# Kernel optimization log

Hardware: AMD Instinct MI355X
Metric: run time of the kernel (lower is better)

Reference implementation:

```python
import jax, jax.numpy as jnp
import numpy as np


def setup_inputs() -> dict:
    key = jax.random.key(0)
    ks = jax.random.split(key, 8)
    C = 256
    x = jax.random.normal(ks[0], (8, C, 64, 64), dtype=jnp.float32)
    scale = 1.0 / np.sqrt(C)
    Wb = jax.random.normal(ks[1], (C, C), dtype=jnp.float32) * scale
    bb = jax.random.normal(ks[2], (C,), dtype=jnp.float32) * 0.01
    Wc = jax.random.normal(ks[3], (C, C), dtype=jnp.float32) * scale
    bc = jax.random.normal(ks[4], (C,), dtype=jnp.float32) * 0.01
    Wd = jax.random.normal(ks[5], (C, C), dtype=jnp.float32) * scale
    bd = jax.random.normal(ks[6], (C,), dtype=jnp.float32) * 0.01
    alpha = jnp.zeros((1,), dtype=jnp.float32) + 0.1  # nonzero so output depends on attention path
    return {"x": x, "Wb": Wb, "bb": bb, "Wc": Wc, "bc": bc, "Wd": Wd, "bd": bd, "alpha": alpha}


def _pam(x, Wb, bb, Wc, bc, Wd, bd, alpha):
    n, c, h, w = x.shape
    xf = x.reshape(n, c, h * w)  # [n, c, N]
    # 1x1 conv == per-pixel linear over channels: W @ x + b
    B = jnp.einsum('oc,ncl->nlo', Wb, xf) + bb  # [n, N, c]
    Cm = jnp.einsum('oc,ncl->nol', Wc, xf) + bc[None, :, None]  # [n, c, N]
    D = jnp.einsum('oc,ncl->nlo', Wd, xf) + bd  # [n, N, c]
    attn = jax.nn.softmax(jnp.einsum('nic,ncj->nij', B, Cm), axis=-1)  # [n, N, N]
    y = jnp.einsum('nij,njc->nic', attn, D)  # [n, N, c]
    y = y.transpose(0, 2, 1).reshape(n, c, h, w)
    return alpha * y + x


def reference(x, Wb, bb, Wc, bc, Wd, bd, alpha):
    return _pam(x, Wb, bb, Wc, bc, Wd, bd, alpha)
```

## Files before the change

kernel.cpp:

```cpp
#include <hip/hip_runtime.h>

using bf16x8 = __attribute__((ext_vector_type(8))) short;
using f32x4  = __attribute__((ext_vector_type(4))) float;
using f32x16 = __attribute__((ext_vector_type(16))) float;
using u32x4  = __attribute__((ext_vector_type(4))) unsigned int;

#define NPIX 4096
#define CCH  256

__device__ __forceinline__ unsigned short f2bf(float f) {
  unsigned int u = __builtin_bit_cast(unsigned int, f);
  u += 0x7FFFu + ((u >> 16) & 1u);
  return (unsigned short)(u >> 16);
}

__device__ __forceinline__ float bfu(unsigned short h) {
  unsigned int u = ((unsigned int)h) << 16;
  return __builtin_bit_cast(float, u);
}

__device__ __forceinline__ unsigned int pack2(float a, float b) {
  return (unsigned int)f2bf(a) | ((unsigned int)f2bf(b) << 16);
}

__device__ __forceinline__ void gld_lds16(const void* g, void* l) {
  __builtin_amdgcn_global_load_lds(
      (const __attribute__((address_space(1))) unsigned int*)g,
      (__attribute__((address_space(3))) unsigned int*)l, 16, 0, 0);
}

__global__ __launch_bounds__(256) void convert_w_kernel(
    const float* __restrict__ Wb, const float* __restrict__ Wc,
    const float* __restrict__ Wd, unsigned short* __restrict__ Wbf) {
  const int mat = blockIdx.y;
  const float* src = (mat == 0) ? Wb : (mat == 1) ? Wc : Wd;
  int i = (blockIdx.x * 256 + threadIdx.x) * 4;
  float4 v = *reinterpret_cast<const float4*>(src + i);
  uint2 o;
  o.x = pack2(v.x, v.y);
  o.y = pack2(v.z, v.w);
  *reinterpret_cast<uint2*>(Wbf + mat * 65536 + i) = o;
}

__global__ __launch_bounds__(256, 2) void fused_proj_kernel(
    const float* __restrict__ x, const unsigned short* __restrict__ Wbf,
    const float* __restrict__ bb, const float* __restrict__ bc,
    const float* __restrict__ bd, unsigned short* __restrict__ Q,
    unsigned short* __restrict__ K, unsigned short* __restrict__ Vt) {
  __shared__ __align__(16) float tile[64][65];
  __shared__ __align__(16) char xsub[32768];
  char* bounce = (char*)tile;

  const int tid = threadIdx.x;
  const int wid = tid >> 6, lane = tid & 63;
  const int l31 = lane & 31, hi = lane >> 5;
  const int lt = blockIdx.x, n = blockIdx.y;

  #pragma unroll 1
  for (int ct = 0; ct < 4; ++ct) {
    const float* xg = x + ((size_t)(n * CCH + ct * 64)) * NPIX + lt * 64;
    #pragma unroll
    for (int it = 0; it < 4; ++it) {
      int row = (tid >> 4) + it * 16;
      int col = (tid & 15) * 4;
      float4 v = *reinterpret_cast<const float4*>(xg + (size_t)row * NPIX + col);
      tile[row][col] = v.x; tile[row][col + 1] = v.y;
      tile[row][col + 2] = v.z; tile[row][col + 3] = v.w;
    }
    __syncthreads();
    #pragma unroll
    for (int it = 0; it < 2; ++it) {
      int idx = tid + it * 256;
      int l = idx >> 3;
      int ch = (idx & 7) * 8;
      int c = ct * 64 + ch;
      uint4 o;
      o.x = pack2(tile[ch + 0][l], tile[ch + 1][l]);
      o.y = pack2(tile[ch + 2][l], tile[ch + 3][l]);
      o.z = pack2(tile[ch + 4][l], tile[ch + 5][l]);
      o.w = pack2(tile[ch + 6][l], tile[ch + 7][l]);
      int addr = (l >> 5) * 16384 + (c >> 4) * 1024 + ((c >> 3) & 1) * 512 + (l & 31) * 16;
      *reinterpret_cast<uint4*>(xsub + addr) = o;
    }
    __syncthreads();
  }

  const int o0a = wid * 64, o0b = wid * 64 + 32;
  const size_t pixrow = (size_t)n * NPIX + lt * 64;

  #pragma unroll 1
  for (int mat = 0; mat < 3; ++mat) {
    const unsigned short* W = Wbf + mat * 65536;
    const float* bias = (mat == 0) ? bb : (mat == 1) ? bc : bd;
    f32x16 a00, a01, a10, a11;
    #pragma unroll
    for (int e = 0; e < 16; ++e) { a00[e] = 0.f; a01[e] = 0.f; a10[e] = 0.f; a11[e] = 0.f; }
    #pragma unroll
    for (int c0 = 0; c0 < 16; ++c0) {
      bf16x8 x0 = *reinterpret_cast<const bf16x8*>(xsub + c0 * 1024 + lane * 16);
      bf16x8 x1 = *reinterpret_cast<const bf16x8*>(xsub + 16384 + c0 * 1024 + lane * 16);
      bf16x8 w0 = *reinterpret_cast<const bf16x8*>(W + (o0a + l31) * CCH + c0 * 16 + hi * 8);
      bf16x8 w1 = *reinterpret_cast<const bf16x8*>(W + (o0b + l31) * CCH + c0 * 16 + hi * 8);
      if (mat < 2) {
        a00 = __builtin_amdgcn_mfma_f32_32x32x16_bf16(w0, x0, a00, 0, 0, 0);
        a01 = __builtin_amdgcn_mfma_f32_32x32x16_bf16(w0, x1, a01, 0, 0, 0);
        a10 = __builtin_amdgcn_mfma_f32_32x32x16_bf16(w1, x0, a10, 0, 0, 0);
        a11 = __builtin_amdgcn_mfma_f32_32x32x16_bf16(w1, x1, a11, 0, 0, 0);
      } else {
        a00 = __builtin_amdgcn_mfma_f32_32x32x16_bf16(x0, w0, a00, 0, 0, 0);
        a01 = __builtin_amdgcn_mfma_f32_32x32x16_bf16(x1, w0, a01, 0, 0, 0);
        a10 = __builtin_amdgcn_mfma_f32_32x32x16_bf16(x0, w1, a10, 0, 0, 0);
        a11 = __builtin_amdgcn_mfma_f32_32x32x16_bf16(x1, w1, a11, 0, 0, 0);
      }
    }
    if (mat < 2) {
      unsigned short* dst = (mat == 0) ? Q : K;
      #pragma unroll 1
      for (int ph = 0; ph < 2; ++ph) {
        __syncthreads();
        const f32x16& A0 = ph ? a01 : a00;
        const f32x16& A1 = ph ? a11 : a10;
        const int swz = (l31 & 15) << 4;
        #pragma unroll
        for (int r2 = 0; r2 < 8; ++r2) {
          const int r = r2 * 2;
          const int od = (r & 3) + 8 * (r >> 2) + 4 * hi;
          const int oa = o0a + od, ob = o0b + od;
          *reinterpret_cast<unsigned int*>(bounce + ((l31 * 512 + oa * 2) ^ swz)) =
              pack2(A0[r] + bias[oa], A0[r + 1] + bias[oa + 1]);
          *reinterpret_cast<unsigned int*>(bounce + ((l31 * 512 + ob * 2) ^ swz)) =
              pack2(A1[r] + bias[ob], A1[r + 1] + bias[ob + 1]);
        }
        __syncthreads();
        const int dp = tid >> 3, obase = (tid & 7) * 32;
        const int dswz = (dp & 15) << 4;
        char* gout = (char*)(dst + (pixrow + ph * 32 + dp) * CCH + obase);
        #pragma unroll
        for (int k = 0; k < 4; ++k) {
          u32x4 v = *reinterpret_cast<const u32x4*>(
              bounce + ((dp * 512 + obase * 2 + k * 16) ^ dswz));
          *reinterpret_cast<u32x4*>(gout + k * 16) = v;
        }
      }
    } else {
      #pragma unroll 1
      for (int os = 0; os < 2; ++os) {
        __syncthreads();
        if ((wid >> 1) == os) {
          const int ola = o0a + l31 - os * 128, olb = o0b + l31 - os * 128;
          const float bva = bias[o0a + l31], bvb = bias[o0b + l31];
          const int sza = (ola & 7) << 4, szb = (olb & 7) << 4;
          #pragma unroll
          for (int r2 = 0; r2 < 8; ++r2) {
            const int r = r2 * 2;
            const int pd = (r & 3) + 8 * (r >> 2) + 4 * hi;
            *reinterpret_cast<unsigned int*>(bounce + ((ola * 128 + pd * 2) ^ sza)) =
                pack2(a00[r] + bva, a00[r + 1] + bva);
            *reinterpret_cast<unsigned int*>(bounce + ((ola * 128 + (pd + 32) * 2) ^ sza)) =
                pack2(a01[r] + bva, a01[r + 1] + bva);
            *reinterpret_cast<unsigned int*>(bounce + ((olb * 128 + pd * 2) ^ szb)) =
                pack2(a10[r] + bvb, a10[r + 1] + bvb);
            *reinterpret_cast<unsigned int*>(bounce + ((olb * 128 + (pd + 32) * 2) ^ szb)) =
                pack2(a11[r] + bvb, a11[r + 1] + bvb);
          }
        }
        __syncthreads();
        const int ol = tid >> 1, pb0 = (tid & 1) * 32;
        const int vswz = (ol & 7) << 4;
        char* gout = (char*)(Vt + ((size_t)(n * CCH + os * 128 + ol)) * NPIX + lt * 64 + pb0);
        #pragma unroll
        for (int k = 0; k < 4; ++k) {
          u32x4 v = *reinterpret_cast<const u32x4*>(
              bounce + ((ol * 128 + pb0 * 2 + k * 16) ^ vswz));
          *reinterpret_cast<u32x4*>(gout + k * 16) = v;
        }
      }
    }
  }
}

__global__ __launch_bounds__(256, 2) void attn_part_kernel(
    const unsigned short* __restrict__ Q, const unsigned short* __restrict__ K,
    const unsigned short* __restrict__ Vt, unsigned short* __restrict__ Opart,
    float* __restrict__ lsumbuf) {
  __shared__ __align__(16) char smem[65536];

  const int tid = threadIdx.x;
  const int wid = tid >> 6;
  const int lane = tid & 63;
  const int l31 = lane & 31;
  const int hi = lane >> 5;
  const int lofs = lane << 4;
  const int blk = blockIdx.x;
  const int n = blk & 7;
  const int t2 = blk >> 3;
  const int half = t2 & 1;
  const int qb = t2 >> 1;
  const int q0 = qb * 128 + wid * 32;

  const unsigned short* Qg = Q + (size_t)n * NPIX * CCH;
  const char* Kg = (const char*)(K + ((size_t)n * NPIX + half * 2048) * CCH);
  const char* Vg = (const char*)(Vt + (size_t)n * CCH * NPIX + half * 2048);

  bf16x8 qf[16];
  #pragma unroll
  for (int c0 = 0; c0 < 16; ++c0)
    qf[c0] = *reinterpret_cast<const bf16x8*>(
        Qg + (size_t)(q0 + l31) * CCH + c0 * 16 + hi * 8);

  f32x16 oacc[8];
  #pragma unroll
  for (int i = 0; i < 8; ++i)
    #pragma unroll
    for (int e = 0; e < 16; ++e) oacc[i][e] = 0.f;
  float lsum = 0.f;

  const bool isK = wid < 2;
  const char* splane = isK ? Kg : Vg;
  const int sinc = isK ? 32 * 512 : 64;
  int soff[8];
  #pragma unroll
  for (int g = 0; g < 8; ++g) {
    int s = ((wid & 1) << 3) + g;
    if (isK) {
      soff[g] = l31 * 512 + s * 32 + hi * 16;
    } else {
      int cb = s >> 1, kk2 = s & 1;
      soff[g] = (cb * 32 + l31) * 8192 + (kk2 * 16 + hi * 8) * 2;
    }
  }

  auto STAGE = [&](int par, int adv) {
    #pragma unroll
    for (int g = 0; g < 8; ++g)
      gld_lds16(splane + (size_t)soff[g] + (size_t)adv,
                smem + par * 32768 + (((wid << 3) + g) << 10));
  };

  STAGE(0, 0);
  __syncthreads();

  #pragma unroll 1
  for (int t = 0; t < 64; ++t) {
    const int par = t & 1;
    const char* kb = smem + par * 32768;
    const char* vb = kb + 16384;

    f32x16 S;
    #pragma unroll
    for (int e = 0; e < 16; ++e) S[e] = 0.f;
    __builtin_amdgcn_s_setprio(1);
    #pragma unroll
    for (int c0 = 0; c0 < 16; ++c0) {
      bf16x8 kf = *reinterpret_cast<const bf16x8*>(kb + c0 * 1024 + lofs);
      S = __builtin_amdgcn_mfma_f32_32x32x16_bf16(kf, qf[c0], S, 0, 0, 0);
    }
    __builtin_amdgcn_s_setprio(0);

    if (t < 63) STAGE(par ^ 1, (t + 1) * sinc);

    float rsum = 0.f;
    unsigned int pw[8];
    #pragma unroll
    for (int i = 0; i < 8; ++i) {
      float p0 = exp2f(fmaf(S[2 * i],     1.44269504f, -101.0f));
      float p1 = exp2f(fmaf(S[2 * i + 1], 1.44269504f, -101.0f));
      rsum += p0 + p1;
      unsigned int r;
      asm("v_cvt_pk_bf16_f32 %0, %1, %2" : "=v"(r) : "v"(p0), "v"(p1));
      pw[i] = r;
    }
    lsum += rsum;

    unsigned int s0a = pw[0], s0b = pw[2];
    unsigned int s1a = pw[1], s1b = pw[3];
    unsigned int s2a = pw[4], s2b = pw[6];
    unsigned int s3a = pw[5], s3b = pw[7];
    asm volatile("v_permlane32_swap_b32 %0, %1" : "+v"(s0a), "+v"(s0b));
    asm volatile("v_permlane32_swap_b32 %0, %1" : "+v"(s1a), "+v"(s1b));
    asm volatile("v_permlane32_swap_b32 %0, %1" : "+v"(s2a), "+v"(s2b));
    asm volatile("v_permlane32_swap_b32 %0, %1" : "+v"(s3a), "+v"(s3b));
    u32x4 f0, f1;
    f0[0] = s0a; f0[1] = s1a; f0[2] = s0b; f0[3] = s1b;
    f1[0] = s2a; f1[1] = s3a; f1[2] = s2b; f1[3] = s3b;
    bf16x8 pa0 = __builtin_bit_cast(bf16x8, f0);
    bf16x8 pa1 = __builtin_bit_cast(bf16x8, f1);

    __builtin_amdgcn_s_setprio(1);
    #pragma unroll
    for (int cb = 0; cb < 8; ++cb) {
      bf16x8 v0 = *reinterpret_cast<const bf16x8*>(vb + (cb * 2 + 0) * 1024 + lofs);
      oacc[cb] = __builtin_amdgcn_mfma_f32_32x32x16_bf16(pa0, v0, oacc[cb], 0, 0, 0);
      bf16x8 v1 = *reinterpret_cast<const bf16x8*>(vb + (cb * 2 + 1) * 1024 + lofs);
      oacc[cb] = __builtin_amdgcn_mfma_f32_32x32x16_bf16(pa1, v1, oacc[cb], 0, 0, 0);
    }
    __builtin_amdgcn_s_setprio(0);

    __syncthreads();
  }

  lsum += __shfl_xor(lsum, 32);
  char* slab = (char*)Opart + (size_t)blk * 65536;
  #pragma unroll
  for (int cb = 0; cb < 8; ++cb) {
    u32x4 u0, u1;
    u0[0] = pack2(oacc[cb][0],  oacc[cb][1]);
    u0[1] = pack2(oacc[cb][2],  oacc[cb][3]);
    u0[2] = pack2(oacc[cb][4],  oacc[cb][5]);
    u0[3] = pack2(oacc[cb][6],  oacc[cb][7]);
    u1[0] = pack2(oacc[cb][8],  oacc[cb][9]);
    u1[1] = pack2(oacc[cb][10], oacc[cb][11]);
    u1[2] = pack2(oacc[cb][12], oacc[cb][13]);
    u1[3] = pack2(oacc[cb][14], oacc[cb][15]);
    *reinterpret_cast<u32x4*>(slab + (cb * 2 + 0) * 4096 + tid * 16) = u0;
    *reinterpret_cast<u32x4*>(slab + (cb * 2 + 1) * 4096 + tid * 16) = u1;
  }
  if (hi == 0) lsumbuf[blk * 128 + wid * 32 + l31] = lsum;
}

__global__ __launch_bounds__(512) void merge_kernel(
    const unsigned short* __restrict__ Opart, const float* __restrict__ lsumbuf,
    const float* __restrict__ x, const float* __restrict__ alpha_p,
    float* __restrict__ out) {
  __shared__ float T[32768];
  __shared__ float Lq[128];

  const int tid = threadIdx.x;
  const int pr8 = tid >> 6;
  const int lane = tid & 63;
  const int l31 = lane & 31;
  const int hi = lane >> 5;
  const int qsub = pr8 & 3;
  const int cbh = pr8 >> 2;
  const int atid = qsub * 64 + lane;
  const int m = blockIdx.x;
  const int n = m & 7;
  const int qb = m >> 3;
  const int blkA = n + 8 * (0 + 2 * qb);
  const int blkB = n + 8 * (1 + 2 * qb);

  if (tid < 128)
    Lq[tid] = alpha_p[0] / (lsumbuf[blkA * 128 + tid] + lsumbuf[blkB * 128 + tid]);
  __syncthreads();

  const char* sa = (const char*)Opart + (size_t)blkA * 65536;
  const char* sb = (const char*)Opart + (size_t)blkB * 65536;

  #pragma unroll
  for (int cbi = 0; cbi < 4; ++cbi) {
    const int cb = cbh * 4 + cbi;
    const int c = cb * 32 + l31;
    const int swz = c & 28;
    #pragma unroll
    for (int h = 0; h < 2; ++h) {
      u32x4 a = *reinterpret_cast<const u32x4*>(sa + (cb * 2 + h) * 4096 + atid * 16);
      u32x4 b = *reinterpret_cast<const u32x4*>(sb + (cb * 2 + h) * 4096 + atid * 16);
      #pragma unroll
      for (int w = 0; w < 4; ++w) {
        const int r = h * 8 + w * 2;
        float v0 = bfu((unsigned short)(a[w] & 0xFFFF)) + bfu((unsigned short)(b[w] & 0xFFFF));
        float v1 = bfu((unsigned short)(a[w] >> 16)) + bfu((unsigned short)(b[w] >> 16));
        const int q0l = qsub * 32 + ((r) & 3) + 8 * ((r) >> 2) + 4 * hi;
        const int q1l = q0l + 1;
        T[c * 128 + (q0l ^ swz)] = v0 * Lq[q0l];
        T[c * 128 + (q1l ^ swz)] = v1 * Lq[q1l];
      }
    }
  }
  __syncthreads();

  const int l0 = (tid & 31) * 4;
  #pragma unroll 4
  for (int sw = 0; sw < 16; ++sw) {
    const int c = (tid >> 5) + sw * 16;
    const float* src = &T[c * 128 + (l0 ^ (c & 28))];
    float4 v = *reinterpret_cast<const float4*>(src);
    const size_t g = ((size_t)n * CCH + c) * NPIX + qb * 128 + l0;
    float4 xi = *reinterpret_cast<const float4*>(x + g);
    float4 o;
    o.x = v.x + xi.x; o.y = v.y + xi.y; o.z = v.z + xi.z; o.w = v.w + xi.w;
    *reinterpret_cast<float4*>(out + g) = o;
  }
}

extern "C" void kernel_launch(void* const* d_in, const int* in_sizes, int n_in,
                              void* d_out, int out_size, void* d_ws, size_t ws_size,
                              hipStream_t stream) {
  const float* x  = (const float*)d_in[0];
  const float* Wb = (const float*)d_in[1];
  const float* bb = (const float*)d_in[2];
  const float* Wc = (const float*)d_in[3];
  const float* bc = (const float*)d_in[4];
  const float* Wd = (const float*)d_in[5];
  const float* bd = (const float*)d_in[6];
  const float* alpha = (const float*)d_in[7];
  float* out = (float*)d_out;
  char* ws = (char*)d_ws;

  unsigned short* Wbf   = (unsigned short*)(ws);
  unsigned short* Q     = (unsigned short*)(ws + 393216);
  unsigned short* K     = (unsigned short*)(ws + 17170432);
  unsigned short* Vt    = (unsigned short*)(ws + 33947648);
  unsigned short* Opart = (unsigned short*)(ws + 50724864);
  float*          lsumb = (float*)(ws + 84279296);

  convert_w_kernel<<<dim3(64, 3), 256, 0, stream>>>(Wb, Wc, Wd, Wbf);
  fused_proj_kernel<<<dim3(64, 8), 256, 0, stream>>>(x, Wbf, bb, bc, bd, Q, K, Vt);
  attn_part_kernel<<<dim3(512), 256, 0, stream>>>(Q, K, Vt, Opart, lsumb);
  merge_kernel<<<dim3(256), 512, 0, stream>>>(Opart, lsumb, x, alpha, out);
}
```

Measured before the change: 215.1 us.

## Split K/V staging across all waves with finer-grained vmcnt pipelining

Every wave now loads a share of both the K and the V tiles, instead of two waves loading K and two loading V. The next tile's K is prefetched at the top of each iteration and its V after the QK MFMAs. The single end-of-iteration __syncthreads is replaced by two s_waitcnt vmcnt(8) plus s_barrier points placed just before QK and just before PV, so each phase waits only for the data it consumes. This aims to overlap global-to-LDS transfers more deeply with compute, at the cost of one redundant wrapped tile load per block and an extra barrier per iteration.

```diff
diff --git a/kernel.cpp b/kernel.cpp
--- a/kernel.cpp
+++ b/kernel.cpp
@@ -215,36 +215,43 @@
     for (int e = 0; e < 16; ++e) oacc[i][e] = 0.f;
   float lsum = 0.f;
 
-  const bool isK = wid < 2;
-  const char* splane = isK ? Kg : Vg;
-  const int sinc = isK ? 32 * 512 : 64;
-  int soff[8];
+  int soffK[4], soffV[4];
   #pragma unroll
-  for (int g = 0; g < 8; ++g) {
-    int s = ((wid & 1) << 3) + g;
-    if (isK) {
-      soff[g] = l31 * 512 + s * 32 + hi * 16;
-    } else {
-      int cb = s >> 1, kk2 = s & 1;
-      soff[g] = (cb * 32 + l31) * 8192 + (kk2 * 16 + hi * 8) * 2;
-    }
-  }
-
-  auto STAGE = [&](int par, int adv) {
-    #pragma unroll
-    for (int g = 0; g < 8; ++g)
-      gld_lds16(splane + (size_t)soff[g] + (size_t)adv,
-                smem + par * 32768 + (((wid << 3) + g) << 10));
+  for (int g = 0; g < 4; ++g) {
+    const int s = wid * 4 + g;
+    soffK[g] = l31 * 512 + s * 32 + hi * 16;
+    const int cb = s >> 1, kk2 = s & 1;
+    soffV[g] = (cb * 32 + l31) * 8192 + (kk2 * 16 + hi * 8) * 2;
+  }
+
+  auto STAGE_K = [&](int par_, int adv) {
+    #pragma unroll
+    for (int g = 0; g < 4; ++g)
+      gld_lds16(Kg + (size_t)soffK[g] + (size_t)adv,
+                smem + par_ * 32768 + (wid * 4 + g) * 1024);
   };
-
-  STAGE(0, 0);
-  __syncthreads();
+  auto STAGE_V = [&](int par_, int adv) {
+    #pragma unroll
+    for (int g = 0; g < 4; ++g)
+      gld_lds16(Vg + (size_t)soffV[g] + (size_t)adv,
+                smem + par_ * 32768 + 16384 + (wid * 4 + g) * 1024);
+  };
+
+  STAGE_K(0, 0);
+  STAGE_V(0, 0);
 
   #pragma unroll 1
   for (int t = 0; t < 64; ++t) {
     const int par = t & 1;
     const char* kb = smem + par * 32768;
     const char* vb = kb + 16384;
+    const int tn = (t + 1) & 63;
+
+    STAGE_K(par ^ 1, tn * 16384);
+    __builtin_amdgcn_sched_barrier(0);
+    asm volatile("s_waitcnt vmcnt(8)" ::: "memory");
+    __builtin_amdgcn_s_barrier();
+    __builtin_amdgcn_sched_barrier(0);
 
     f32x16 S;
     #pragma unroll
@@ -257,7 +264,7 @@
     }
     __builtin_amdgcn_s_setprio(0);
 
-    if (t < 63) STAGE(par ^ 1, (t + 1) * sinc);
+    STAGE_V(par ^ 1, tn * 64);
 
     float rsum = 0.f;
     unsigned int pw[8];
@@ -286,6 +293,11 @@
     bf16x8 pa0 = __builtin_bit_cast(bf16x8, f0);
     bf16x8 pa1 = __builtin_bit_cast(bf16x8, f1);
 
+    __builtin_amdgcn_sched_barrier(0);
+    asm volatile("s_waitcnt vmcnt(8)" ::: "memory");
+    __builtin_amdgcn_s_barrier();
+    __builtin_amdgcn_sched_barrier(0);
+
     __builtin_amdgcn_s_setprio(1);
     #pragma unroll
     for (int cb = 0; cb < 8; ++cb) {
@@ -295,9 +307,9 @@
       oacc[cb] = __builtin_amdgcn_mfma_f32_32x32x16_bf16(pa1, v1, oacc[cb], 0, 0, 0);
     }
     __builtin_amdgcn_s_setprio(0);
-
-    __syncthreads();
-  }
+  }
+
+  asm volatile("s_waitcnt vmcnt(0)" ::: "memory");
 
   lsum += __shfl_xor(lsum, 32);
   char* slab = (char*)Opart + (size_t)blk * 65536;
```

After: 218.9 us. Within noise of the previous version (+1.7%).
